# Kernel tuning notes

Hardware: AMD Instinct MI355X
Metric: run time of the kernel (lower is better)

Reference implementation:

```python
import jax, jax.numpy as jnp
import numpy as np

N = 100000       # num_nodes
E = 1600000      # num_edges (avg degree 16)
EL = 200000      # link-prediction edges
IN_C = 64
POS = 16
HID = 64
OUT = 32


def setup_inputs() -> dict:
    key = jax.random.key(0)
    ks = jax.random.split(key, 10)
    def glorot(k, shape):
        scale = 1.0 / np.sqrt(shape[0])
        return jax.random.uniform(k, shape, jnp.float32, -scale, scale)
    return {
        "x": jax.random.normal(ks[0], (N, IN_C), jnp.float32),
        "pos_emb": jax.random.normal(ks[1], (N, POS), jnp.float32),
        "W1": glorot(ks[2], (IN_C + POS, HID)),
        "b1": jnp.zeros((HID,), jnp.float32),
        "W2": glorot(ks[3], (HID, OUT)),
        "b2": jnp.zeros((OUT,), jnp.float32),
        "Wl": glorot(ks[4], (2 * OUT, 1)),
        "bl": jnp.zeros((1,), jnp.float32),
        "edge_index": jax.random.randint(ks[5], (2, E), 0, N, jnp.int32),
        "edge_label_index": jax.random.randint(ks[6], (2, EL), 0, N, jnp.int32),
    }


def reference(x, pos_emb, W1, b1, W2, b2, Wl, bl, edge_index, edge_label_index):
    n = x.shape[0]
    # GCNConv: add self-loops, symmetric deg^{-1/2} normalization (PyG defaults)
    loops = jnp.arange(n, dtype=edge_index.dtype)
    src = jnp.concatenate([edge_index[0], loops])  # [E+N]
    dst = jnp.concatenate([edge_index[1], loops])  # [E+N]
    deg = jax.ops.segment_sum(jnp.ones_like(dst, jnp.float32), dst, num_segments=n)
    dinv = jnp.where(deg > 0, jax.lax.rsqrt(jnp.maximum(deg, 1e-12)), 0.0)
    norm = dinv[src] * dinv[dst]  # [E+N]

    def gcn_conv(h, W, b):
        hw = h @ W                                    # [N, d_out] transform first
        msg = hw[src] * norm[:, None]                 # gather + normalize
        return jax.ops.segment_sum(msg, dst, num_segments=n) + b  # scatter-add

    h = jnp.concatenate([x, pos_emb], axis=1)         # [N, in+pos]
    h = jax.nn.relu(gcn_conv(h, W1, b1))              # dropout is eval no-op
    z = gcn_conv(h, W2, b2)                           # [N, out]

    s, d = edge_label_index[0], edge_label_index[1]
    zc = jnp.concatenate([z[s], z[d]], axis=1)        # [EL, 2*out]
    edge_pred = (zc @ Wl + bl)[:, 0]                  # [EL]
    return z, edge_pred
```

## Files before the change

kernel.cpp:

```cpp
#include <hip/hip_runtime.h>
#include <hip/hip_fp16.h>

#define NN 100000
#define NE 1600000
#define NEL 200000
#define TM 64

#define NBUCK 196
#define CAPB  10240
#define TPE   8192

__global__ __launch_bounds__(256) void k_part(const int* __restrict__ src,
                                              const int* __restrict__ dst,
                                              int* __restrict__ gcur,
                                              int* __restrict__ part) {
    __shared__ int hist[NBUCK];
    __shared__ int base[NBUCK];
    __shared__ int rk[NBUCK];
    int tid = threadIdx.x;
    for (int i = tid; i < NBUCK; i += 256) { hist[i] = 0; rk[i] = 0; }
    __syncthreads();
    int e0 = blockIdx.x * TPE;
    int e1 = min(e0 + TPE, NE);
    for (int e = e0 + tid; e < e1; e += 256)
        atomicAdd(&hist[dst[e] >> 9], 1);
    __syncthreads();
    for (int i = tid; i < NBUCK; i += 256)
        base[i] = i * CAPB + atomicAdd(&gcur[i], hist[i]);
    __syncthreads();
    for (int e = e0 + tid; e < e1; e += 256) {
        int d = dst[e];
        int s = src[e];
        int b = d >> 9;
        int r = atomicAdd(&rk[b], 1);
        part[base[b] + r] = ((d & 511) << 17) | s;
    }
}

__global__ __launch_bounds__(256) void k_build(const int* __restrict__ gcur,
                                               const int* __restrict__ part,
                                               int* __restrict__ csr,
                                               int* __restrict__ off,
                                               float* __restrict__ dinv) {
    __shared__ int cnts[256];
    __shared__ int hist[512];
    __shared__ int loff[512];
    __shared__ int ssum[256];
    __shared__ int csrbuf[CAPB];
    int b = blockIdx.x;
    int tid = threadIdx.x;
    cnts[tid] = (tid < NBUCK) ? gcur[tid] : 0;
    __syncthreads();
    for (int st = 1; st < 256; st <<= 1) {
        int tmp = (tid >= st) ? cnts[tid - st] : 0;
        __syncthreads();
        cnts[tid] += tmp;
        __syncthreads();
    }
    int obase = (b == 0) ? 0 : cnts[b - 1];
    int cnt = gcur[b];
    int pbase = b * CAPB;
    hist[tid] = 0; hist[tid + 256] = 0;
    __syncthreads();
    for (int i = tid; i < cnt; i += 256)
        atomicAdd(&hist[part[pbase + i] >> 17], 1);
    __syncthreads();
    int a0 = hist[2 * tid], a1 = hist[2 * tid + 1];
    int pairs = a0 + a1;
    ssum[tid] = pairs;
    __syncthreads();
    for (int st = 1; st < 256; st <<= 1) {
        int tmp = (tid >= st) ? ssum[tid - st] : 0;
        __syncthreads();
        ssum[tid] += tmp;
        __syncthreads();
    }
    int pexcl = ssum[tid] - pairs;
    loff[2 * tid] = pexcl;
    loff[2 * tid + 1] = pexcl + a0;
    __syncthreads();
    for (int i = tid; i < 512; i += 256) {
        int d = b * 512 + i;
        if (d < NN) {
            int c = hist[i];
            off[d] = obase + loff[i] + c;
            dinv[d] = rsqrtf((float)(c + 1));
        }
    }
    hist[tid] = 0; hist[tid + 256] = 0;
    __syncthreads();
    for (int i = tid; i < cnt; i += 256) {
        int rec = part[pbase + i];
        int dl = rec >> 17;
        int r = atomicAdd(&hist[dl], 1);
        csrbuf[loff[dl] + r] = rec & 0x1FFFF;
    }
    __syncthreads();
    for (int i = tid; i < cnt; i += 256)
        csr[obase + i] = csrbuf[i];
}

__global__ __launch_bounds__(256) void k_hw1(const float* __restrict__ x,
                                             const float* __restrict__ pos,
                                             const float* __restrict__ W1,
                                             const float* __restrict__ dinv,
                                             __half* __restrict__ hw1) {
    __shared__ float sh[TM * 80];
    __shared__ float sw[80 * 64];
    int tid = threadIdx.x;
    for (int t = tid; t < 80 * 64; t += 256) sw[t] = W1[t];
    int nb = blockIdx.x * TM;
    for (int i = tid; i < TM * 64; i += 256) {
        int node = i >> 6, ch = i & 63;
        int g = nb + node;
        sh[node * 80 + ch] = (g < NN) ? x[g * 64 + ch] : 0.0f;
    }
    for (int i = tid; i < TM * 16; i += 256) {
        int node = i >> 4, ch = i & 15;
        int g = nb + node;
        sh[node * 80 + 64 + ch] = (g < NN) ? pos[g * 16 + ch] : 0.0f;
    }
    __syncthreads();
    int j  = (tid & 15) * 4;
    int nl = (tid >> 4) * 4;
    float a00=0,a01=0,a02=0,a03=0, a10=0,a11=0,a12=0,a13=0;
    float a20=0,a21=0,a22=0,a23=0, a30=0,a31=0,a32=0,a33=0;
#pragma unroll 4
    for (int k = 0; k < 80; ++k) {
        float4 wv = *(const float4*)&sw[k * 64 + j];
        float h0 = sh[(nl + 0) * 80 + k];
        float h1 = sh[(nl + 1) * 80 + k];
        float h2 = sh[(nl + 2) * 80 + k];
        float h3 = sh[(nl + 3) * 80 + k];
        a00 += h0 * wv.x; a01 += h0 * wv.y; a02 += h0 * wv.z; a03 += h0 * wv.w;
        a10 += h1 * wv.x; a11 += h1 * wv.y; a12 += h1 * wv.z; a13 += h1 * wv.w;
        a20 += h2 * wv.x; a21 += h2 * wv.y; a22 += h2 * wv.z; a23 += h2 * wv.w;
        a30 += h3 * wv.x; a31 += h3 * wv.y; a32 += h3 * wv.z; a33 += h3 * wv.w;
    }
    int g0 = nb + nl;
    union { __half2 h2v[2]; float2 f2; } u;
#define STORE_ROW(r, b0, b1, b2, b3)                                          \
    if (g0 + r < NN) {                                                        \
        float sc = dinv[g0 + r];                                              \
        u.h2v[0] = __floats2half2_rn(b0 * sc, b1 * sc);                       \
        u.h2v[1] = __floats2half2_rn(b2 * sc, b3 * sc);                       \
        *(float2*)&hw1[(g0 + r) * 64 + j] = u.f2;                             \
    }
    STORE_ROW(0, a00, a01, a02, a03)
    STORE_ROW(1, a10, a11, a12, a13)
    STORE_ROW(2, a20, a21, a22, a23)
    STORE_ROW(3, a30, a31, a32, a33)
#undef STORE_ROW
}

__global__ __launch_bounds__(256) void k_gather1(const int* __restrict__ off,
                                                 const int* __restrict__ csr,
                                                 const float* __restrict__ dinv,
                                                 const __half* __restrict__ hw,
                                                 const float* __restrict__ b1,
                                                 const float* __restrict__ W2,
                                                 __half* __restrict__ hw2out) {
    __shared__ float w[64 * 32];
    for (int t = threadIdx.x; t < 64 * 32; t += 256) w[t] = W2[t];
    __syncthreads();
    int lane = threadIdx.x & 63;
    int wave = threadIdx.x >> 6;
    int d = blockIdx.x * 4 + wave;
    int start = (d == 0) ? 0 : off[d - 1];
    int end = off[d];
    start = __builtin_amdgcn_readfirstlane(start);
    end   = __builtin_amdgcn_readfirstlane(end);
    float dd = dinv[d];
    float hself = __half2float(hw[d * 64 + lane]);
    float acc0 = 0.0f, acc1 = 0.0f, acc2 = 0.0f, acc3 = 0.0f;
    int e = start;
    for (; e + 7 < end; e += 8) {
        int s0 = csr[e],     s1 = csr[e + 1];
        int s2 = csr[e + 2], s3 = csr[e + 3];
        int s4 = csr[e + 4], s5 = csr[e + 5];
        int s6 = csr[e + 6], s7 = csr[e + 7];
        float g0 = __half2float(hw[s0 * 64 + lane]);
        float g1 = __half2float(hw[s1 * 64 + lane]);
        float g2 = __half2float(hw[s2 * 64 + lane]);
        float g3 = __half2float(hw[s3 * 64 + lane]);
        float g4 = __half2float(hw[s4 * 64 + lane]);
        float g5 = __half2float(hw[s5 * 64 + lane]);
        float g6 = __half2float(hw[s6 * 64 + lane]);
        float g7 = __half2float(hw[s7 * 64 + lane]);
        acc0 += g0; acc1 += g1; acc2 += g2; acc3 += g3;
        acc0 += g4; acc1 += g5; acc2 += g6; acc3 += g7;
    }
    for (; e < end; ++e)
        acc0 += __half2float(hw[csr[e] * 64 + lane]);
    float v = fmaxf(b1[lane] + dd * (((acc0 + acc1) + (acc2 + acc3)) + hself), 0.0f);
    int j = lane & 31;
    int base2 = (lane >> 5) << 5;
    float acc = 0.0f;
#pragma unroll 8
    for (int k = 0; k < 32; ++k)
        acc += __shfl(v, base2 + k, 64) * w[(base2 + k) * 32 + j];
    acc += __shfl(acc, lane ^ 32, 64);
    if (lane < 32) hw2out[d * 32 + j] = __float2half_rn(acc * dd);
}

__global__ __launch_bounds__(256) void k_gather2(const int* __restrict__ off,
                                                 const int* __restrict__ csr,
                                                 const float* __restrict__ dinv,
                                                 const __half* __restrict__ hw,
                                                 const float* __restrict__ b2,
                                                 float* __restrict__ outz) {
    int lane = threadIdx.x & 63;
    int half = lane >> 5;
    int j = lane & 31;
    int wave = threadIdx.x >> 6;
    int d = blockIdx.x * 4 + wave;
    int start = (d == 0) ? 0 : off[d - 1];
    int end = off[d];
    start = __builtin_amdgcn_readfirstlane(start);
    end   = __builtin_amdgcn_readfirstlane(end);
    float dd = dinv[d];
    float hself = __half2float(hw[d * 32 + j]);
    float accA = 0.0f, accB = 0.0f, accC = 0.0f, accD = 0.0f;
    int e = start;
    for (; e + 7 < end; e += 8) {
        int sA = csr[e + half];
        int sB = csr[e + half + 2];
        int sC = csr[e + half + 4];
        int sD = csr[e + half + 6];
        accA += __half2float(hw[sA * 32 + j]);
        accB += __half2float(hw[sB * 32 + j]);
        accC += __half2float(hw[sC * 32 + j]);
        accD += __half2float(hw[sD * 32 + j]);
    }
    for (int ee = e + half; ee < end; ee += 2)
        accA += __half2float(hw[csr[ee] * 32 + j]);
    float acc = (accA + accB) + (accC + accD);
    acc += __shfl(acc, lane ^ 32, 64);
    if (half == 0)
        outz[d * 32 + j] = b2[j] + dd * (acc + hself);
}

__global__ __launch_bounds__(256) void k_linkpred(const int* __restrict__ sidx,
                                                  const int* __restrict__ didx,
                                                  const float* __restrict__ z,
                                                  const float* __restrict__ Wl,
                                                  const float* __restrict__ bl,
                                                  float* __restrict__ pred) {
    int t = blockIdx.x * blockDim.x + threadIdx.x;
    int e = t >> 4;
    int l = t & 15;
    int s = sidx[e], d = didx[e];
    float2 zs = *(const float2*)&z[s * 32 + 2 * l];
    float2 zd = *(const float2*)&z[d * 32 + 2 * l];
    float2 ws = *(const float2*)&Wl[2 * l];
    float2 wd = *(const float2*)&Wl[32 + 2 * l];
    float v = zs.x * ws.x + zs.y * ws.y + zd.x * wd.x + zd.y * wd.y;
    v += __shfl_xor(v, 1, 64);
    v += __shfl_xor(v, 2, 64);
    v += __shfl_xor(v, 4, 64);
    v += __shfl_xor(v, 8, 64);
    if (l == 0) pred[e] = v + bl[0];
}

extern "C" void kernel_launch(void* const* d_in, const int* in_sizes, int n_in,
                              void* d_out, int out_size, void* d_ws, size_t ws_size,
                              hipStream_t stream) {
    const float* x    = (const float*)d_in[0];
    const float* pos  = (const float*)d_in[1];
    const float* W1   = (const float*)d_in[2];
    const float* b1   = (const float*)d_in[3];
    const float* W2   = (const float*)d_in[4];
    const float* b2   = (const float*)d_in[5];
    const float* Wl   = (const float*)d_in[6];
    const float* bl   = (const float*)d_in[7];
    const int*   ei   = (const int*)d_in[8];
    const int*   eli  = (const int*)d_in[9];
    const int* src  = ei;
    const int* dst  = ei + NE;
    const int* lsrc = eli;
    const int* ldst = eli + NEL;

    float* out_z    = (float*)d_out;
    float* out_pred = (float*)d_out + NN * 32;

    float*  dinv  = (float*)d_ws;
    int*    off   = (int*)(dinv + NN);
    int*    gcur  = off + NN;
    int*    csr   = gcur + NBUCK;
    __half* hw1   = (__half*)(csr + NE);
    int*    part  = (int*)hw1;
    __half* hw2   = hw1 + NN * 64;

    hipMemsetAsync(gcur, 0, NBUCK * sizeof(int), stream);
    k_part<<<(NE + TPE - 1) / TPE, 256, 0, stream>>>(src, dst, gcur, part);
    k_build<<<NBUCK, 256, 0, stream>>>(gcur, part, csr, off, dinv);

    k_hw1<<<(NN + TM - 1) / TM, 256, 0, stream>>>(x, pos, W1, dinv, hw1);

    k_gather1<<<NN / 4, 256, 0, stream>>>(off, csr, dinv, hw1, b1, W2, hw2);

    k_gather2<<<NN / 4, 256, 0, stream>>>(off, csr, dinv, hw2, b2, out_z);

    k_linkpred<<<NEL * 16 / 256, 256, 0, stream>>>(lsrc, ldst, out_z, Wl, bl, out_pred);
}
```

Baseline: 314.1 us.

## Fuse all GCN stages into one cooperative persistent kernel with grid syncs

Replaces the six separate launches and the memset with a single cooperative persistent kernel that runs each stage in grid-stride loops separated by grid-wide barriers. The CSR build now scatters straight to global memory instead of staging in shared memory. The layer-2 transform is split out of the first gather into its own tiled matmul, which costs an extra fp16 hidden buffer round trip. W1 is stored in shared memory as fp16. The aim is to remove launch overhead and tail gaps between stages, at the cost of grid-sync latency and occupancy fixed by the persistent grid.

```diff
diff --git a/kernel.cpp b/kernel.cpp
--- a/kernel.cpp
+++ b/kernel.cpp
@@ -1,265 +1,296 @@
 #include <hip/hip_runtime.h>
 #include <hip/hip_fp16.h>
+#include <hip/hip_cooperative_groups.h>
+
+namespace cg = cooperative_groups;
 
 #define NN 100000
 #define NE 1600000
 #define NEL 200000
-#define TM 64
 
 #define NBUCK 196
 #define CAPB  10240
 #define TPE   8192
-
-__global__ __launch_bounds__(256) void k_part(const int* __restrict__ src,
-                                              const int* __restrict__ dst,
-                                              int* __restrict__ gcur,
-                                              int* __restrict__ part) {
-    __shared__ int hist[NBUCK];
-    __shared__ int base[NBUCK];
-    __shared__ int rk[NBUCK];
-    int tid = threadIdx.x;
-    for (int i = tid; i < NBUCK; i += 256) { hist[i] = 0; rk[i] = 0; }
-    __syncthreads();
-    int e0 = blockIdx.x * TPE;
-    int e1 = min(e0 + TPE, NE);
-    for (int e = e0 + tid; e < e1; e += 256)
-        atomicAdd(&hist[dst[e] >> 9], 1);
-    __syncthreads();
-    for (int i = tid; i < NBUCK; i += 256)
-        base[i] = i * CAPB + atomicAdd(&gcur[i], hist[i]);
-    __syncthreads();
-    for (int e = e0 + tid; e < e1; e += 256) {
-        int d = dst[e];
-        int s = src[e];
-        int b = d >> 9;
-        int r = atomicAdd(&rk[b], 1);
-        part[base[b] + r] = ((d & 511) << 17) | s;
-    }
-}
-
-__global__ __launch_bounds__(256) void k_build(const int* __restrict__ gcur,
-                                               const int* __restrict__ part,
-                                               int* __restrict__ csr,
-                                               int* __restrict__ off,
-                                               float* __restrict__ dinv) {
-    __shared__ int cnts[256];
-    __shared__ int hist[512];
-    __shared__ int loff[512];
-    __shared__ int ssum[256];
-    __shared__ int csrbuf[CAPB];
-    int b = blockIdx.x;
-    int tid = threadIdx.x;
-    cnts[tid] = (tid < NBUCK) ? gcur[tid] : 0;
-    __syncthreads();
-    for (int st = 1; st < 256; st <<= 1) {
-        int tmp = (tid >= st) ? cnts[tid - st] : 0;
-        __syncthreads();
-        cnts[tid] += tmp;
-        __syncthreads();
-    }
-    int obase = (b == 0) ? 0 : cnts[b - 1];
-    int cnt = gcur[b];
-    int pbase = b * CAPB;
-    hist[tid] = 0; hist[tid + 256] = 0;
-    __syncthreads();
-    for (int i = tid; i < cnt; i += 256)
-        atomicAdd(&hist[part[pbase + i] >> 17], 1);
-    __syncthreads();
-    int a0 = hist[2 * tid], a1 = hist[2 * tid + 1];
-    int pairs = a0 + a1;
-    ssum[tid] = pairs;
-    __syncthreads();
-    for (int st = 1; st < 256; st <<= 1) {
-        int tmp = (tid >= st) ? ssum[tid - st] : 0;
-        __syncthreads();
-        ssum[tid] += tmp;
-        __syncthreads();
-    }
-    int pexcl = ssum[tid] - pairs;
-    loff[2 * tid] = pexcl;
-    loff[2 * tid + 1] = pexcl + a0;
-    __syncthreads();
-    for (int i = tid; i < 512; i += 256) {
-        int d = b * 512 + i;
-        if (d < NN) {
-            int c = hist[i];
-            off[d] = obase + loff[i] + c;
-            dinv[d] = rsqrtf((float)(c + 1));
-        }
-    }
-    hist[tid] = 0; hist[tid + 256] = 0;
-    __syncthreads();
-    for (int i = tid; i < cnt; i += 256) {
-        int rec = part[pbase + i];
-        int dl = rec >> 17;
-        int r = atomicAdd(&hist[dl], 1);
-        csrbuf[loff[dl] + r] = rec & 0x1FFFF;
-    }
-    __syncthreads();
-    for (int i = tid; i < cnt; i += 256)
-        csr[obase + i] = csrbuf[i];
-}
-
-__global__ __launch_bounds__(256) void k_hw1(const float* __restrict__ x,
-                                             const float* __restrict__ pos,
-                                             const float* __restrict__ W1,
-                                             const float* __restrict__ dinv,
-                                             __half* __restrict__ hw1) {
-    __shared__ float sh[TM * 80];
-    __shared__ float sw[80 * 64];
-    int tid = threadIdx.x;
-    for (int t = tid; t < 80 * 64; t += 256) sw[t] = W1[t];
-    int nb = blockIdx.x * TM;
-    for (int i = tid; i < TM * 64; i += 256) {
-        int node = i >> 6, ch = i & 63;
-        int g = nb + node;
-        sh[node * 80 + ch] = (g < NN) ? x[g * 64 + ch] : 0.0f;
-    }
-    for (int i = tid; i < TM * 16; i += 256) {
-        int node = i >> 4, ch = i & 15;
-        int g = nb + node;
-        sh[node * 80 + 64 + ch] = (g < NN) ? pos[g * 16 + ch] : 0.0f;
-    }
-    __syncthreads();
-    int j  = (tid & 15) * 4;
-    int nl = (tid >> 4) * 4;
-    float a00=0,a01=0,a02=0,a03=0, a10=0,a11=0,a12=0,a13=0;
-    float a20=0,a21=0,a22=0,a23=0, a30=0,a31=0,a32=0,a33=0;
+#define NT1   1563
+#define NT2   1563
+#define NU_G  25000
+#define NU_LP 12500
+
+union SharedU {
+    struct { int hist[NBUCK], base[NBUCK], rk[NBUCK]; } part;
+    struct { int cnts[256]; int hist[512]; int loff[512]; int ssum[256]; } build;
+    struct { float sh[64 * 81]; __half sw[80 * 64]; } hw1;
+    struct { float sh[64 * 65]; float sw[64 * 32]; } hw2;
+};
+
+__global__ __launch_bounds__(256, 4) void k_mega(
+        const int* __restrict__ src, const int* __restrict__ dst,
+        const float* __restrict__ x, const float* __restrict__ pos,
+        const float* __restrict__ W1, const float* __restrict__ b1,
+        const float* __restrict__ W2, const float* __restrict__ b2,
+        const float* __restrict__ Wl, const float* __restrict__ bl,
+        const int* __restrict__ lsrc, const int* __restrict__ ldst,
+        int* __restrict__ gcur, int* __restrict__ part,
+        int* __restrict__ csr, int* __restrict__ off,
+        float* __restrict__ dinv, __half* __restrict__ hw1,
+        __half* __restrict__ h2buf, __half* __restrict__ hw2,
+        float* __restrict__ outz, float* __restrict__ pred)
+{
+    cg::grid_group grid = cg::this_grid();
+    __shared__ SharedU S;
+    int tid  = threadIdx.x;
+    int bid  = blockIdx.x;
+    int nblk = gridDim.x;
+    int lane = tid & 63;
+    int wave = tid >> 6;
+
+    if (bid == 0)
+        for (int i = tid; i < NBUCK; i += 256) gcur[i] = 0;
+    grid.sync();
+
+    for (int tile = bid; tile < NBUCK; tile += nblk) {
+        for (int i = tid; i < NBUCK; i += 256) { S.part.hist[i] = 0; S.part.rk[i] = 0; }
+        __syncthreads();
+        int e0 = tile * TPE;
+        int e1 = min(e0 + TPE, NE);
+        for (int e = e0 + tid; e < e1; e += 256)
+            atomicAdd(&S.part.hist[dst[e] >> 9], 1);
+        __syncthreads();
+        for (int i = tid; i < NBUCK; i += 256)
+            S.part.base[i] = i * CAPB + atomicAdd(&gcur[i], S.part.hist[i]);
+        __syncthreads();
+        for (int e = e0 + tid; e < e1; e += 256) {
+            int d = dst[e];
+            int s = src[e];
+            int b = d >> 9;
+            int r = atomicAdd(&S.part.rk[b], 1);
+            part[S.part.base[b] + r] = ((d & 511) << 17) | s;
+        }
+        __syncthreads();
+    }
+    grid.sync();
+
+    for (int b = bid; b < NBUCK; b += nblk) {
+        S.build.cnts[tid] = (tid < NBUCK) ? gcur[tid] : 0;
+        __syncthreads();
+        for (int st = 1; st < 256; st <<= 1) {
+            int tmp = (tid >= st) ? S.build.cnts[tid - st] : 0;
+            __syncthreads();
+            S.build.cnts[tid] += tmp;
+            __syncthreads();
+        }
+        int obase = (b == 0) ? 0 : S.build.cnts[b - 1];
+        int cnt = gcur[b];
+        int pbase = b * CAPB;
+        S.build.hist[tid] = 0; S.build.hist[tid + 256] = 0;
+        __syncthreads();
+        for (int i = tid; i < cnt; i += 256)
+            atomicAdd(&S.build.hist[part[pbase + i] >> 17], 1);
+        __syncthreads();
+        int a0 = S.build.hist[2 * tid], a1 = S.build.hist[2 * tid + 1];
+        int pairs = a0 + a1;
+        S.build.ssum[tid] = pairs;
+        __syncthreads();
+        for (int st = 1; st < 256; st <<= 1) {
+            int tmp = (tid >= st) ? S.build.ssum[tid - st] : 0;
+            __syncthreads();
+            S.build.ssum[tid] += tmp;
+            __syncthreads();
+        }
+        int pexcl = S.build.ssum[tid] - pairs;
+        S.build.loff[2 * tid] = pexcl;
+        S.build.loff[2 * tid + 1] = pexcl + a0;
+        __syncthreads();
+        for (int i = tid; i < 512; i += 256) {
+            int d = b * 512 + i;
+            if (d < NN) {
+                int c = S.build.hist[i];
+                off[d] = obase + S.build.loff[i] + c;
+                dinv[d] = rsqrtf((float)(c + 1));
+            }
+        }
+        S.build.hist[tid] = 0; S.build.hist[tid + 256] = 0;
+        __syncthreads();
+        for (int i = tid; i < cnt; i += 256) {
+            int rec = part[pbase + i];
+            int dl = rec >> 17;
+            int r = atomicAdd(&S.build.hist[dl], 1);
+            csr[obase + S.build.loff[dl] + r] = rec & 0x1FFFF;
+        }
+        __syncthreads();
+    }
+    grid.sync();
+
+    for (int t = tid; t < 80 * 64; t += 256)
+        S.hw1.sw[t] = __float2half(W1[t]);
+    for (int tile = bid; tile < NT1; tile += nblk) {
+        __syncthreads();
+        int nb = tile * 64;
+        for (int i = tid; i < 64 * 64; i += 256) {
+            int node = i >> 6, ch = i & 63;
+            int g = nb + node;
+            S.hw1.sh[node * 81 + ch] = (g < NN) ? x[g * 64 + ch] : 0.0f;
+        }
+        for (int i = tid; i < 64 * 16; i += 256) {
+            int node = i >> 4, ch = i & 15;
+            int g = nb + node;
+            S.hw1.sh[node * 81 + 64 + ch] = (g < NN) ? pos[g * 16 + ch] : 0.0f;
+        }
+        __syncthreads();
+        int j  = (tid & 15) * 4;
+        int nl = (tid >> 4) * 4;
+        float a00=0,a01=0,a02=0,a03=0, a10=0,a11=0,a12=0,a13=0;
+        float a20=0,a21=0,a22=0,a23=0, a30=0,a31=0,a32=0,a33=0;
 #pragma unroll 4
-    for (int k = 0; k < 80; ++k) {
-        float4 wv = *(const float4*)&sw[k * 64 + j];
-        float h0 = sh[(nl + 0) * 80 + k];
-        float h1 = sh[(nl + 1) * 80 + k];
-        float h2 = sh[(nl + 2) * 80 + k];
-        float h3 = sh[(nl + 3) * 80 + k];
-        a00 += h0 * wv.x; a01 += h0 * wv.y; a02 += h0 * wv.z; a03 += h0 * wv.w;
-        a10 += h1 * wv.x; a11 += h1 * wv.y; a12 += h1 * wv.z; a13 += h1 * wv.w;
-        a20 += h2 * wv.x; a21 += h2 * wv.y; a22 += h2 * wv.z; a23 += h2 * wv.w;
-        a30 += h3 * wv.x; a31 += h3 * wv.y; a32 += h3 * wv.z; a33 += h3 * wv.w;
-    }
-    int g0 = nb + nl;
-    union { __half2 h2v[2]; float2 f2; } u;
+        for (int k = 0; k < 80; ++k) {
+            float2 wr = *(const float2*)&S.hw1.sw[k * 64 + j];
+            __half2 wA = *(__half2*)&wr.x;
+            __half2 wB = *(__half2*)&wr.y;
+            float2 wAf = __half22float2(wA);
+            float2 wBf = __half22float2(wB);
+            float h0 = S.hw1.sh[(nl + 0) * 81 + k];
+            float h1 = S.hw1.sh[(nl + 1) * 81 + k];
+            float h2 = S.hw1.sh[(nl + 2) * 81 + k];
+            float h3 = S.hw1.sh[(nl + 3) * 81 + k];
+            a00 += h0 * wAf.x; a01 += h0 * wAf.y; a02 += h0 * wBf.x; a03 += h0 * wBf.y;
+            a10 += h1 * wAf.x; a11 += h1 * wAf.y; a12 += h1 * wBf.x; a13 += h1 * wBf.y;
+            a20 += h2 * wAf.x; a21 += h2 * wAf.y; a22 += h2 * wBf.x; a23 += h2 * wBf.y;
+            a30 += h3 * wAf.x; a31 += h3 * wAf.y; a32 += h3 * wBf.x; a33 += h3 * wBf.y;
+        }
+        int g0 = nb + nl;
+        union { __half2 hv[2]; float2 f2; } u;
 #define STORE_ROW(r, b0, b1, b2, b3)                                          \
-    if (g0 + r < NN) {                                                        \
-        float sc = dinv[g0 + r];                                              \
-        u.h2v[0] = __floats2half2_rn(b0 * sc, b1 * sc);                       \
-        u.h2v[1] = __floats2half2_rn(b2 * sc, b3 * sc);                       \
-        *(float2*)&hw1[(g0 + r) * 64 + j] = u.f2;                             \
-    }
-    STORE_ROW(0, a00, a01, a02, a03)
-    STORE_ROW(1, a10, a11, a12, a13)
-    STORE_ROW(2, a20, a21, a22, a23)
-    STORE_ROW(3, a30, a31, a32, a33)
+        if (g0 + r < NN) {                                                    \
+            float sc = dinv[g0 + r];                                          \
+            u.hv[0] = __floats2half2_rn(b0 * sc, b1 * sc);                    \
+            u.hv[1] = __floats2half2_rn(b2 * sc, b3 * sc);                    \
+            *(float2*)&hw1[(g0 + r) * 64 + j] = u.f2;                         \
+        }
+        STORE_ROW(0, a00, a01, a02, a03)
+        STORE_ROW(1, a10, a11, a12, a13)
+        STORE_ROW(2, a20, a21, a22, a23)
+        STORE_ROW(3, a30, a31, a32, a33)
 #undef STORE_ROW
-}
-
-__global__ __launch_bounds__(256) void k_gather1(const int* __restrict__ off,
-                                                 const int* __restrict__ csr,
-                                                 const float* __restrict__ dinv,
-                                                 const __half* __restrict__ hw,
-                                                 const float* __restrict__ b1,
-                                                 const float* __restrict__ W2,
-                                                 __half* __restrict__ hw2out) {
-    __shared__ float w[64 * 32];
-    for (int t = threadIdx.x; t < 64 * 32; t += 256) w[t] = W2[t];
-    __syncthreads();
-    int lane = threadIdx.x & 63;
-    int wave = threadIdx.x >> 6;
-    int d = blockIdx.x * 4 + wave;
-    int start = (d == 0) ? 0 : off[d - 1];
-    int end = off[d];
-    start = __builtin_amdgcn_readfirstlane(start);
-    end   = __builtin_amdgcn_readfirstlane(end);
-    float dd = dinv[d];
-    float hself = __half2float(hw[d * 64 + lane]);
-    float acc0 = 0.0f, acc1 = 0.0f, acc2 = 0.0f, acc3 = 0.0f;
-    int e = start;
-    for (; e + 7 < end; e += 8) {
-        int s0 = csr[e],     s1 = csr[e + 1];
-        int s2 = csr[e + 2], s3 = csr[e + 3];
-        int s4 = csr[e + 4], s5 = csr[e + 5];
-        int s6 = csr[e + 6], s7 = csr[e + 7];
-        float g0 = __half2float(hw[s0 * 64 + lane]);
-        float g1 = __half2float(hw[s1 * 64 + lane]);
-        float g2 = __half2float(hw[s2 * 64 + lane]);
-        float g3 = __half2float(hw[s3 * 64 + lane]);
-        float g4 = __half2float(hw[s4 * 64 + lane]);
-        float g5 = __half2float(hw[s5 * 64 + lane]);
-        float g6 = __half2float(hw[s6 * 64 + lane]);
-        float g7 = __half2float(hw[s7 * 64 + lane]);
-        acc0 += g0; acc1 += g1; acc2 += g2; acc3 += g3;
-        acc0 += g4; acc1 += g5; acc2 += g6; acc3 += g7;
-    }
-    for (; e < end; ++e)
-        acc0 += __half2float(hw[csr[e] * 64 + lane]);
-    float v = fmaxf(b1[lane] + dd * (((acc0 + acc1) + (acc2 + acc3)) + hself), 0.0f);
-    int j = lane & 31;
-    int base2 = (lane >> 5) << 5;
-    float acc = 0.0f;
-#pragma unroll 8
-    for (int k = 0; k < 32; ++k)
-        acc += __shfl(v, base2 + k, 64) * w[(base2 + k) * 32 + j];
-    acc += __shfl(acc, lane ^ 32, 64);
-    if (lane < 32) hw2out[d * 32 + j] = __float2half_rn(acc * dd);
-}
-
-__global__ __launch_bounds__(256) void k_gather2(const int* __restrict__ off,
-                                                 const int* __restrict__ csr,
-                                                 const float* __restrict__ dinv,
-                                                 const __half* __restrict__ hw,
-                                                 const float* __restrict__ b2,
-                                                 float* __restrict__ outz) {
-    int lane = threadIdx.x & 63;
-    int half = lane >> 5;
-    int j = lane & 31;
-    int wave = threadIdx.x >> 6;
-    int d = blockIdx.x * 4 + wave;
-    int start = (d == 0) ? 0 : off[d - 1];
-    int end = off[d];
-    start = __builtin_amdgcn_readfirstlane(start);
-    end   = __builtin_amdgcn_readfirstlane(end);
-    float dd = dinv[d];
-    float hself = __half2float(hw[d * 32 + j]);
-    float accA = 0.0f, accB = 0.0f, accC = 0.0f, accD = 0.0f;
-    int e = start;
-    for (; e + 7 < end; e += 8) {
-        int sA = csr[e + half];
-        int sB = csr[e + half + 2];
-        int sC = csr[e + half + 4];
-        int sD = csr[e + half + 6];
-        accA += __half2float(hw[sA * 32 + j]);
-        accB += __half2float(hw[sB * 32 + j]);
-        accC += __half2float(hw[sC * 32 + j]);
-        accD += __half2float(hw[sD * 32 + j]);
-    }
-    for (int ee = e + half; ee < end; ee += 2)
-        accA += __half2float(hw[csr[ee] * 32 + j]);
-    float acc = (accA + accB) + (accC + accD);
-    acc += __shfl(acc, lane ^ 32, 64);
-    if (half == 0)
-        outz[d * 32 + j] = b2[j] + dd * (acc + hself);
-}
-
-__global__ __launch_bounds__(256) void k_linkpred(const int* __restrict__ sidx,
-                                                  const int* __restrict__ didx,
-                                                  const float* __restrict__ z,
-                                                  const float* __restrict__ Wl,
-                                                  const float* __restrict__ bl,
-                                                  float* __restrict__ pred) {
-    int t = blockIdx.x * blockDim.x + threadIdx.x;
-    int e = t >> 4;
-    int l = t & 15;
-    int s = sidx[e], d = didx[e];
-    float2 zs = *(const float2*)&z[s * 32 + 2 * l];
-    float2 zd = *(const float2*)&z[d * 32 + 2 * l];
-    float2 ws = *(const float2*)&Wl[2 * l];
-    float2 wd = *(const float2*)&Wl[32 + 2 * l];
-    float v = zs.x * ws.x + zs.y * ws.y + zd.x * wd.x + zd.y * wd.y;
-    v += __shfl_xor(v, 1, 64);
-    v += __shfl_xor(v, 2, 64);
-    v += __shfl_xor(v, 4, 64);
-    v += __shfl_xor(v, 8, 64);
-    if (l == 0) pred[e] = v + bl[0];
+    }
+    grid.sync();
+
+    for (int u = bid; u < NU_G; u += nblk) {
+        int d = u * 4 + wave;
+        int start = (d == 0) ? 0 : off[d - 1];
+        int end = off[d];
+        start = __builtin_amdgcn_readfirstlane(start);
+        end   = __builtin_amdgcn_readfirstlane(end);
+        float dd = dinv[d];
+        float hself = __half2float(hw1[d * 64 + lane]);
+        float acc0 = 0.0f, acc1 = 0.0f, acc2 = 0.0f, acc3 = 0.0f;
+        int e = start;
+        for (; e + 7 < end; e += 8) {
+            int s0 = csr[e],     s1 = csr[e + 1];
+            int s2 = csr[e + 2], s3 = csr[e + 3];
+            int s4 = csr[e + 4], s5 = csr[e + 5];
+            int s6 = csr[e + 6], s7 = csr[e + 7];
+            float g0 = __half2float(hw1[s0 * 64 + lane]);
+            float g1 = __half2float(hw1[s1 * 64 + lane]);
+            float g2 = __half2float(hw1[s2 * 64 + lane]);
+            float g3 = __half2float(hw1[s3 * 64 + lane]);
+            float g4 = __half2float(hw1[s4 * 64 + lane]);
+            float g5 = __half2float(hw1[s5 * 64 + lane]);
+            float g6 = __half2float(hw1[s6 * 64 + lane]);
+            float g7 = __half2float(hw1[s7 * 64 + lane]);
+            acc0 += g0; acc1 += g1; acc2 += g2; acc3 += g3;
+            acc0 += g4; acc1 += g5; acc2 += g6; acc3 += g7;
+        }
+        for (; e < end; ++e)
+            acc0 += __half2float(hw1[csr[e] * 64 + lane]);
+        float v = fmaxf(b1[lane] + dd * (((acc0 + acc1) + (acc2 + acc3)) + hself), 0.0f);
+        h2buf[d * 64 + lane] = __float2half_rn(v);
+    }
+    grid.sync();
+
+    for (int t = tid; t < 64 * 32; t += 256)
+        S.hw2.sw[t] = W2[t];
+    for (int tile = bid; tile < NT2; tile += nblk) {
+        __syncthreads();
+        int nb = tile * 64;
+        for (int i = tid; i < 64 * 64; i += 256) {
+            int node = i >> 6, ch = i & 63;
+            int g = nb + node;
+            S.hw2.sh[node * 65 + ch] = (g < NN) ? __half2float(h2buf[g * 64 + ch]) : 0.0f;
+        }
+        __syncthreads();
+        int j  = (tid & 7) * 4;
+        int nl = (tid >> 3) * 2;
+        float a00=0,a01=0,a02=0,a03=0, a10=0,a11=0,a12=0,a13=0;
+#pragma unroll 4
+        for (int k = 0; k < 64; ++k) {
+            float4 wv = *(const float4*)&S.hw2.sw[k * 32 + j];
+            float h0 = S.hw2.sh[(nl + 0) * 65 + k];
+            float h1 = S.hw2.sh[(nl + 1) * 65 + k];
+            a00 += h0 * wv.x; a01 += h0 * wv.y; a02 += h0 * wv.z; a03 += h0 * wv.w;
+            a10 += h1 * wv.x; a11 += h1 * wv.y; a12 += h1 * wv.z; a13 += h1 * wv.w;
+        }
+        int g0 = nb + nl;
+        union { __half2 hv[2]; float2 f2; } u;
+#define STORE_ROW2(r, b0, b1, b2, b3)                                         \
+        if (g0 + r < NN) {                                                    \
+            float sc = dinv[g0 + r];                                          \
+            u.hv[0] = __floats2half2_rn(b0 * sc, b1 * sc);                    \
+            u.hv[1] = __floats2half2_rn(b2 * sc, b3 * sc);                    \
+            *(float2*)&hw2[(g0 + r) * 32 + j] = u.f2;                         \
+        }
+        STORE_ROW2(0, a00, a01, a02, a03)
+        STORE_ROW2(1, a10, a11, a12, a13)
+#undef STORE_ROW2
+    }
+    grid.sync();
+
+    for (int u = bid; u < NU_G; u += nblk) {
+        int d = u * 4 + wave;
+        int half = lane >> 5;
+        int j = lane & 31;
+        int start = (d == 0) ? 0 : off[d - 1];
+        int end = off[d];
+        start = __builtin_amdgcn_readfirstlane(start);
+        end   = __builtin_amdgcn_readfirstlane(end);
+        float dd = dinv[d];
+        float hself = __half2float(hw2[d * 32 + j]);
+        float accA = 0.0f, accB = 0.0f, accC = 0.0f, accD = 0.0f;
+        int e = start;
+        for (; e + 7 < end; e += 8) {
+            int sA = csr[e + half];
+            int sB = csr[e + half + 2];
+            int sC = csr[e + half + 4];
+            int sD = csr[e + half + 6];
+            accA += __half2float(hw2[sA * 32 + j]);
+            accB += __half2float(hw2[sB * 32 + j]);
+            accC += __half2float(hw2[sC * 32 + j]);
+            accD += __half2float(hw2[sD * 32 + j]);
+        }
+        for (int ee = e + half; ee < end; ee += 2)
+            accA += __half2float(hw2[csr[ee] * 32 + j]);
+        float acc = (accA + accB) + (accC + accD);
+        acc += __shfl(acc, lane ^ 32, 64);
+        if (half == 0)
+            outz[d * 32 + j] = b2[j] + dd * (acc + hself);
+    }
+    grid.sync();
+
+    for (int u = bid; u < NU_LP; u += nblk) {
+        int g = u * 256 + tid;
+        int e = g >> 4;
+        int l = g & 15;
+        int s = lsrc[e], d = ldst[e];
+        float2 zs = *(const float2*)&outz[s * 32 + 2 * l];
+        float2 zd = *(const float2*)&outz[d * 32 + 2 * l];
+        float2 ws = *(const float2*)&Wl[2 * l];
+        float2 wd = *(const float2*)&Wl[32 + 2 * l];
+        float v = zs.x * ws.x + zs.y * ws.y + zd.x * wd.x + zd.y * wd.y;
+        v += __shfl_xor(v, 1, 64);
+        v += __shfl_xor(v, 2, 64);
+        v += __shfl_xor(v, 4, 64);
+        v += __shfl_xor(v, 8, 64);
+        if (l == 0) pred[e] = v + bl[0];
+    }
 }
 
 extern "C" void kernel_launch(void* const* d_in, const int* in_sizes, int n_in,
@@ -289,17 +320,20 @@
     int*    csr   = gcur + NBUCK;
     __half* hw1   = (__half*)(csr + NE);
     int*    part  = (int*)hw1;
-    __half* hw2   = hw1 + NN * 64;
-
-    hipMemsetAsync(gcur, 0, NBUCK * sizeof(int), stream);
-    k_part<<<(NE + TPE - 1) / TPE, 256, 0, stream>>>(src, dst, gcur, part);
-    k_build<<<NBUCK, 256, 0, stream>>>(gcur, part, csr, off, dinv);
-
-    k_hw1<<<(NN + TM - 1) / TM, 256, 0, stream>>>(x, pos, W1, dinv, hw1);
-
-    k_gather1<<<NN / 4, 256, 0, stream>>>(off, csr, dinv, hw1, b1, W2, hw2);
-
-    k_gather2<<<NN / 4, 256, 0, stream>>>(off, csr, dinv, hw2, b2, out_z);
-
-    k_linkpred<<<NEL * 16 / 256, 256, 0, stream>>>(lsrc, ldst, out_z, Wl, bl, out_pred);
+    __half* h2    = hw1 + NN * 64;
+    __half* hw2   = h2 + NN * 64;
+
+    int occ = 0;
+    hipOccupancyMaxActiveBlocksPerMultiprocessor(&occ, k_mega, 256, 0);
+    if (occ < 1) occ = 1;
+    int nblk = occ * 256;
+
+    void* args[] = { (void*)&src, (void*)&dst, (void*)&x, (void*)&pos,
+                     (void*)&W1, (void*)&b1, (void*)&W2, (void*)&b2,
+                     (void*)&Wl, (void*)&bl, (void*)&lsrc, (void*)&ldst,
+                     (void*)&gcur, (void*)&part, (void*)&csr, (void*)&off,
+                     (void*)&dinv, (void*)&hw1, (void*)&h2, (void*)&hw2,
+                     (void*)&out_z, (void*)&out_pred };
+    hipLaunchCooperativeKernel((const void*)k_mega, dim3(nblk), dim3(256),
+                               args, 0, stream);
 }
```

Measured after the change: 1.003 ms. 219% more time.
